# Optimization experiments

Hardware: AMD Instinct MI355X
Metric: run time of the kernel (lower is better)

## Reference

```python
import jax, jax.numpy as jnp
import numpy as np

B, T, ENC_C = 64, 512, 512   # batch, encoder frames, encoder channels
H = 512                      # hidden_channels
D = 80                       # out_channels (mel dim)
RF = 2                       # reduction_factor
PRE_IN = D * RF              # prenet input (= D*2, see go_frame)
PRE_INNER = 256
CONV_CH = 32                 # location conv channels
K = 31                       # location conv kernel size


def setup_inputs():
    key = jax.random.key(0)
    ks = jax.random.split(key, 16)
    s = 0.02
    f32 = jnp.float32
    p = {}
    p['enc_output'] = jax.random.normal(ks[0], (B, T, ENC_C), f32)
    # acoustic lengths in [T, 2T], multiples of RF -> len//RF in [T//2, T]
    p['data_len'] = (jax.random.randint(ks[1], (B,), T // 2, T + 1, jnp.int32) * RF).astype(jnp.int32)
    # Prenet: two 1x1 convs (== linears) + ReLU
    p['pn_w1'] = jax.random.normal(ks[2], (PRE_INNER, PRE_IN), f32) * s
    p['pn_b1'] = jnp.zeros((PRE_INNER,), f32)
    p['pn_w2'] = jax.random.normal(ks[3], (H, PRE_INNER), f32) * s
    p['pn_b2'] = jnp.zeros((H,), f32)
    # Location-sensitive attention
    p['att_enc_w'] = jax.random.normal(ks[4], (H, ENC_C), f32) * s
    p['att_enc_b'] = jnp.zeros((H,), f32)
    p['att_dec_w'] = jax.random.normal(ks[5], (H, H), f32) * s
    p['att_conv_w'] = jax.random.normal(ks[6], (CONV_CH, 1, K), f32) * s
    p['att_loc_w'] = jax.random.normal(ks[7], (H, CONV_CH), f32) * s
    p['att_v_w'] = jax.random.normal(ks[8], (H,), f32) * s
    p['att_v_b'] = jnp.zeros((), f32)
    # 2 GRU cells (torch GRUCell layout: gates [r|z|n])
    p['gru0_wih'] = jax.random.normal(ks[9], (3 * H, ENC_C + H), f32) * s
    p['gru0_whh'] = jax.random.normal(ks[10], (3 * H, H), f32) * s
    p['gru0_bih'] = jnp.zeros((3 * H,), f32)
    p['gru0_bhh'] = jnp.zeros((3 * H,), f32)
    p['gru1_wih'] = jax.random.normal(ks[11], (3 * H, H), f32) * s
    p['gru1_whh'] = jax.random.normal(ks[12], (3 * H, H), f32) * s
    p['gru1_bih'] = jnp.zeros((3 * H,), f32)
    p['gru1_bhh'] = jnp.zeros((3 * H,), f32)
    # out_layer: 1x1 Conv1d(2H -> D*RF) == linear
    p['out_w'] = jax.random.normal(ks[13], (D * RF, 2 * H), f32) * s
    p['out_b'] = jnp.zeros((D * RF,), f32)
    return p


def _gru(x, h, wih, whh, bih, bhh):
    gi = x @ wih.T + bih
    gh = h @ whh.T + bhh
    ir, iz, inn = jnp.split(gi, 3, axis=-1)
    hr, hz, hn = jnp.split(gh, 3, axis=-1)
    r = jax.nn.sigmoid(ir + hr)
    z = jax.nn.sigmoid(iz + hz)
    n = jnp.tanh(inn + r * hn)
    return (1.0 - z) * n + z * h


def _decode(enc_output, data_len, pn_w1, pn_b1, pn_w2, pn_b2,
            att_enc_w, att_enc_b, att_dec_w, att_conv_w, att_loc_w, att_v_w, att_v_b,
            gru0_wih, gru0_whh, gru0_bih, gru0_bhh,
            gru1_wih, gru1_whh, gru1_bih, gru1_bhh, out_w, out_b):
    dt = enc_output.dtype
    len_r = data_len // RF                                   # (B,) encoder-frame lengths
    pad = jnp.arange(T)[None, :] >= len_r[:, None]           # (B,T) True at padding
    valid = (~pad).astype(dt)
    att_prev0 = valid / len_r.astype(dt)[:, None]            # uniform init attention
    # processed memory (computed once, as in attention.reset_state caching)
    pm = jnp.einsum('btc,hc->bth', enc_output, att_enc_w) + att_enc_b

    def step(carry, t):
        h0, h1, prev_out, att_sum = carry
        prev_w = jnp.where(t == 0, att_prev0, att_sum)       # (B,T)
        # location features: 1D conv over previous (cumulative) attention
        f = jax.lax.conv_general_dilated(prev_w[:, None, :], att_conv_w,
                                         (1,), [(K // 2, K // 2)])  # (B,CONV_CH,T)
        loc = jnp.einsum('bct,hc->bth', f, att_loc_w)
        dec = (h0 @ att_dec_w.T)[:, None, :]                 # query from GRU layer 0 state
        erg = jnp.tanh(loc + pm + dec) @ att_v_w + att_v_b   # (B,T)
        erg = jnp.where(pad, jnp.asarray(-1e9, dt), erg)
        att_w = jax.nn.softmax(erg, axis=-1)
        att_c = jnp.einsum('bt,btc->bc', att_w, enc_output)  # context (B,ENC_C)
        # prenet (dropout in eval == identity)
        x = jax.nn.relu(prev_out @ pn_w1.T + pn_b1)
        x = jax.nn.relu(x @ pn_w2.T + pn_b2)
        h0n = _gru(jnp.concatenate([x, att_c], -1), h0, gru0_wih, gru0_whh, gru0_bih, gru0_bhh)
        h1n = _gru(h0n, h1, gru1_wih, gru1_whh, gru1_bih, gru1_bhh)
        out = jnp.concatenate([h1n, att_c], -1) @ out_w.T + out_b   # (B, D*RF)
        return (h0n, h1n, out, att_sum + att_w), (out, att_w)

    zeros = lambda *s: jnp.zeros(s, dt)
    carry0 = (zeros(B, H), zeros(B, H), zeros(B, D * RF), zeros(B, T))
    _, (outs, att_ws) = jax.lax.scan(step, carry0, jnp.arange(T))
    # outs: (T,B,D*RF); each step reshapes to (B,D,RF) and cats on time
    out = outs.transpose(1, 0, 2).reshape(B, T, D, RF).transpose(0, 2, 1, 3).reshape(B, D, T * RF)
    att_w = att_ws.transpose(1, 2, 0)                        # (B, T, T_steps)
    return out, att_w


def reference(enc_output, data_len, pn_w1, pn_b1, pn_w2, pn_b2,
              att_enc_w, att_enc_b, att_dec_w, att_conv_w, att_loc_w, att_v_w, att_v_b,
              gru0_wih, gru0_whh, gru0_bih, gru0_bhh,
              gru1_wih, gru1_whh, gru1_bih, gru1_bhh, out_w, out_b):
    return _decode(enc_output, data_len, pn_w1, pn_b1, pn_w2, pn_b2,
                   att_enc_w, att_enc_b, att_dec_w, att_conv_w, att_loc_w, att_v_w, att_v_b,
                   gru0_wih, gru0_whh, gru0_bih, gru0_bhh,
                   gru1_wih, gru1_whh, gru1_bih, gru1_bhh, out_w, out_b)
```

## Files before the change

kernel.cpp:

```cpp
#include <hip/hip_runtime.h>
#include <hip/hip_bf16.h>

typedef unsigned short u16;


__device__ __forceinline__ float b2f(u16 u) {
  return __uint_as_float(((unsigned)u) << 16);
}
__device__ __forceinline__ u16 f2b(float f) {
  unsigned u = __float_as_uint(f);
  u += 0x7fffu + ((u >> 16) & 1u);
  return (u16)(u >> 16);
}
template<bool F32>
__device__ __forceinline__ float ldw(const void* p, size_t i) {
  return F32 ? ((const float*)p)[i] : b2f(((const u16*)p)[i]);
}
template<bool F32>
__device__ __forceinline__ float4 ldw4(const void* p, size_t i) {
  if (F32) {
    return *(const float4*)((const float*)p + i);
  } else {
    uint2 u = *(const uint2*)((const u16*)p + i);
    float4 r;
    r.x = __uint_as_float(u.x << 16);
    r.y = __uint_as_float(u.x & 0xffff0000u);
    r.z = __uint_as_float(u.y << 16);
    r.w = __uint_as_float(u.y & 0xffff0000u);
    return r;
  }
}
template<bool F32>
__device__ __forceinline__ void stout(void* p, size_t i, float v) {
  if (F32) ((float*)p)[i] = v; else ((u16*)p)[i] = f2b(v);
}
__device__ __forceinline__ float frcp(float x) { return __builtin_amdgcn_rcpf(x); }
__device__ __forceinline__ float tanh_f(float x) {
  float e = __expf(2.f * x);
  return 1.f - 2.f * frcp(e + 1.f);
}
__device__ __forceinline__ float sig_f(float x) { return frcp(1.f + __expf(-x)); }

__device__ __forceinline__ void st_sc(int* p, int v) {
  __hip_atomic_store(p, v, __ATOMIC_RELAXED, __HIP_MEMORY_SCOPE_AGENT);
}
__device__ __forceinline__ int ld_sc(const int* p) {
  return __hip_atomic_load(p, __ATOMIC_RELAXED, __HIP_MEMORY_SCOPE_AGENT);
}
__device__ __forceinline__ void stf_sc(float* p, float v) {
  __hip_atomic_store(p, v, __ATOMIC_RELAXED, __HIP_MEMORY_SCOPE_AGENT);
}
__device__ __forceinline__ float ldf_sc(const float* p) {
  return __hip_atomic_load(p, __ATOMIC_RELAXED, __HIP_MEMORY_SCOPE_AGENT);
}

__device__ __forceinline__ void stage_n(float* lds, const float* src, int n, int tid) {
  int i = 0;
  for (; i + 8192 <= n; i += 8192) {
    float r[16];
#pragma unroll
    for (int j = 0; j < 16; ++j) r[j] = ldf_sc(src + i + tid + j * 512);
#pragma unroll
    for (int j = 0; j < 16; ++j) lds[i + tid + j * 512] = r[j];
  }
  for (; i < n; i += 2048) {
    float r[4];
#pragma unroll
    for (int j = 0; j < 4; ++j) r[j] = ldf_sc(src + i + tid + j * 512);
#pragma unroll
    for (int j = 0; j < 4; ++j) lds[i + tid + j * 512] = r[j];
  }
}

template<bool F32, int NR>
__device__ __forceinline__ void dotN(float* __restrict__ acc, const float* __restrict__ sb,
                                     const void* __restrict__ wb, size_t rb, int wstride,
                                     int nk, int lane, int vz) {
  float4 wa[NR], wn[NR];
#pragma unroll
  for (int i = 0; i < NR; ++i) wa[i] = ldw4<F32>(wb, rb + (size_t)i * wstride + vz);
  for (int kg = 0; kg < nk; kg += 8) {
#pragma unroll
    for (int i = 0; i < NR; ++i) wn[i] = ldw4<F32>(wb, rb + (size_t)i * wstride + kg + 4 + vz);
    float a0 = sb[(kg + 0) * 64 + lane], a1 = sb[(kg + 1) * 64 + lane],
          a2 = sb[(kg + 2) * 64 + lane], a3 = sb[(kg + 3) * 64 + lane];
#pragma unroll
    for (int i = 0; i < NR; ++i)
      acc[i] = fmaf(wa[i].w, a3, fmaf(wa[i].z, a2, fmaf(wa[i].y, a1, fmaf(wa[i].x, a0, acc[i]))));
    int kn = (kg + 8 < nk) ? kg + 8 : kg;
#pragma unroll
    for (int i = 0; i < NR; ++i) wa[i] = ldw4<F32>(wb, rb + (size_t)i * wstride + kn + vz);
    float b0 = sb[(kg + 4) * 64 + lane], b1 = sb[(kg + 5) * 64 + lane],
          b2 = sb[(kg + 6) * 64 + lane], b3 = sb[(kg + 7) * 64 + lane];
#pragma unroll
    for (int i = 0; i < NR; ++i)
      acc[i] = fmaf(wn[i].w, b3, fmaf(wn[i].z, b2, fmaf(wn[i].y, b1, fmaf(wn[i].x, b0, acc[i]))));
  }
}

constexpr size_t OBAR  = 0;
constexpr size_t OFLG  = OBAR  + 128;
constexpr size_t OASUM = OFLG  + 8192;
constexpr size_t ODEC  = OASUM + 32768;
constexpr size_t OH0   = ODEC  + 32768;
constexpr size_t OH1   = OH0   + 32768;
constexpr size_t OPO   = OH1   + 32768;
constexpr size_t OZEND = OPO   + 10240;
constexpr int    ZERO_SPAN_N = (int)OZEND;
constexpr size_t OPRV  = OZEND;
constexpr size_t OERG  = OPRV  + 32768;
constexpr size_t OX1   = OERG  + 32768;
constexpr size_t OX2   = OX1   + 16384;
constexpr size_t OATTC = OX2   + 32768;
constexpr size_t OMM   = OATTC + 32768;
constexpr size_t OGI0  = OMM   + 16384;
constexpr size_t OGH0  = OGI0  + 393216;
constexpr size_t OGH1  = OGH0  + 196608;
constexpr size_t OGI1  = OGH1  + 196608;
constexpr size_t OPM   = OGI1  + 393216;
constexpr size_t OTOT  = OPM   + 8388608;

__device__ __forceinline__ void fastbar(int* flags, int* gen, int target,
                                        int wg, int tid) {
  __syncthreads();
  if (tid == 0) st_sc(flags + wg * 32, target);
  if (wg == 0) {
    if (tid < 64) {
      int i0 = tid * 4;
      for (;;) {
        int ok = (ld_sc(flags + (i0 + 0) * 32) >= target)
               & (ld_sc(flags + (i0 + 1) * 32) >= target)
               & (ld_sc(flags + (i0 + 2) * 32) >= target)
               & (ld_sc(flags + (i0 + 3) * 32) >= target);
        if (__ballot(ok) == 0xFFFFFFFFFFFFFFFFull) break;
      }
      if (tid == 0) st_sc(gen, target);
    }
    __syncthreads();
  } else {
    if (tid == 0) {
      while (ld_sc(gen) < target) {}
    }
    __syncthreads();
  }
}

__global__ void k_zero(float* p, int n) {
  for (int i = blockIdx.x * 256 + threadIdx.x; i < n; i += gridDim.x * 256) p[i] = 0.f;
}
__global__ void k_detect(int* flag, const u16* probe) {
  if (blockIdx.x != 0 || threadIdx.x != 0) return;
  int sane = 0;
  for (int i = 0; i < 256; i += 2) {
    u16 u = probe[i];
    int e = (u >> 7) & 0xFF;
    if (u == 0 || (e >= 97 && e <= 140)) ++sane;
  }
  *flag = (sane < 96) ? 1 : 0;
}
__global__ void k_prevw(float* prevw, const int* dlen) {
  int b = blockIdx.x;
  int len = dlen[b] >> 1;
  float inv = 1.f / (float)len;
  for (int i = threadIdx.x; i < 512; i += 256)
    prevw[b * 512 + i] = (i < len) ? inv : 0.f;
}
template<bool F32>
__global__ void k_cvtT512(const int* flag, float* dst, const void* src) {
  if (*flag != (F32 ? 1 : 0)) return;
  for (int i = blockIdx.x * 256 + threadIdx.x; i < 262144; i += gridDim.x * 256) {
    int c = i >> 9, h = i & 511;
    dst[i] = ldw<F32>(src, (size_t)h * 512 + c);
  }
}
template<bool F32>
__global__ void k_mmat(const int* flag, float* M, const void* locw, const void* convw) {
  if (*flag != (F32 ? 1 : 0)) return;
  int i = blockIdx.x * 256 + threadIdx.x;
  if (i >= 16384) return;
  int h = i >> 5, k = i & 31;
  float acc = 0.f;
  if (k < 31) {
    for (int c = 0; c < 32; ++c)
      acc = fmaf(ldw<F32>(locw, h * 32 + c), ldw<F32>(convw, c * 31 + k), acc);
  }
  M[i] = acc;
}
template<bool F32>
__global__ __launch_bounds__(256) void k_pm(const int* flag, u16* pm, const void* enc,
                                            const float* encwT, const void* encb) {
  if (*flag != (F32 ? 1 : 0)) return;
  __shared__ float encf[16 * 512];
  int row0 = blockIdx.x * 16;
  int tid = threadIdx.x;
  for (int i = tid; i < 16 * 512; i += 256) {
    int r = i >> 9, c = i & 511;
    encf[i] = ldw<F32>(enc, (size_t)(row0 + r) * 512 + c);
  }
  __syncthreads();
  float a0[16], a1[16];
  float bb0 = ldw<F32>(encb, tid), bb1 = ldw<F32>(encb, tid + 256);
#pragma unroll
  for (int r = 0; r < 16; ++r) { a0[r] = bb0; a1[r] = bb1; }
  for (int c = 0; c < 512; ++c) {
    float w0 = encwT[c * 512 + tid];
    float w1 = encwT[c * 512 + 256 + tid];
#pragma unroll
    for (int r = 0; r < 16; ++r) {
      float a = encf[r * 512 + c];
      a0[r] = fmaf(w0, a, a0[r]);
      a1[r] = fmaf(w1, a, a1[r]);
    }
  }
#pragma unroll
  for (int r = 0; r < 16; ++r) {
    pm[(size_t)(row0 + r) * 512 + tid]       = f2b(a0[r]);
    pm[(size_t)(row0 + r) * 512 + 256 + tid] = f2b(a1[r]);
  }
}

struct KP {
  const void* __restrict__ enc;
  const int* __restrict__ dlen;
  const u16* __restrict__ pm;
  const void* __restrict__ wih0; const void* __restrict__ whh0;
  const void* __restrict__ wih1; const void* __restrict__ whh1;
  const void* __restrict__ adec; const void* __restrict__ outw;
  const void* __restrict__ pnw2; const void* __restrict__ pnw1;
  const void* __restrict__ pnb1; const void* __restrict__ pnb2;
  const void* __restrict__ bih0; const void* __restrict__ bhh0;
  const void* __restrict__ bih1; const void* __restrict__ bhh1;
  const void* __restrict__ outb; const void* __restrict__ vw;
  const float* __restrict__ Mg;
  int* __restrict__ bar;
  int* __restrict__ flags;
  float* __restrict__ asum; float* __restrict__ dec;
  float* __restrict__ h0T;  float* __restrict__ h1T;  float* __restrict__ poT;
  float* __restrict__ prevw; float* __restrict__ erg;
  float* __restrict__ x1T;  float* __restrict__ x2T;  float* __restrict__ attcT;
  float* __restrict__ gi0p; float* __restrict__ gh0p;
  float* __restrict__ gh1p; float* __restrict__ gi1p;
  void* __restrict__ out;
};

template<bool F32>
__global__ __launch_bounds__(512, 2) void k_loop(KP p) {
  if (*(const volatile int*)(p.bar + 64) != (F32 ? 1 : 0)) return;
  __shared__ float stg[16384];
  __shared__ u16  M_u[32 * 512];
  __shared__ float dec_s[512];
  __shared__ float v_s[512];
  __shared__ float wq[160];
  __shared__ float sm[512];
  __shared__ float red[16];

  const int wg = blockIdx.x, tid = threadIdx.x;
  const int lane = tid & 63;
  const int wv = __builtin_amdgcn_readfirstlane(tid >> 6);
  const int b_att = wg >> 2, q = wg & 3, t0 = q * 128;
  const int trow = tid >> 6;
  const int hcol = tid & 63;
  float* dec1 = p.gh0p;
  int* genp = p.bar + 32;
  int bt = 0;
  int vz;
  asm volatile("v_mov_b32 %0, 0" : "=v"(vz));

  for (int i = tid; i < 32 * 512; i += 512) {
    int k = i >> 9, h = i & 511;
    M_u[i] = f2b(p.Mg[h * 32 + k]);
  }
  if (tid < 512) v_s[tid] = ldw<F32>(p.vw, tid);
  __syncthreads();

  for (int t = 0; t < 512; ++t) {
    if (wg < 32) stage_n(stg, p.poT, 10240, tid);
    if (tid < 158) {
      int g = t0 - 15 + tid;
      wq[tid] = (g >= 0 && g < 512) ? ldf_sc(p.prevw + b_att * 512 + g) : 0.f;
    }
    if (tid < 512)
      dec_s[tid] = ldf_sc(p.dec + b_att * 512 + tid) + ldf_sc(dec1 + b_att * 512 + tid);
    __syncthreads();
    if (wg < 32) {
      int n = wg * 8 + wv;
      float a[1] = {0.f};
      dotN<F32, 1>(a, stg, p.pnw1, (size_t)n * 160, 160, 160, lane, vz);
      stf_sc(p.x1T + n * 64 + lane, fmaxf(a[0] + ldw<F32>(p.pnb1, n), 0.f));
    }
    {
      float wreg[46];
#pragma unroll
      for (int i = 0; i < 46; ++i) wreg[i] = wq[trow * 16 + i];
      float acc[16];
#pragma unroll
      for (int s = 0; s < 16; ++s) acc[s] = 0.f;
      const u16* pmb = p.pm + ((size_t)(b_att * 512 + t0 + trow * 16)) * 512;
      for (int j = 0; j < 8; ++j) {
        int hj = hcol + 64 * j;
        float Mreg[31];
#pragma unroll
        for (int k = 0; k < 31; ++k) Mreg[k] = b2f(M_u[k * 512 + hj]);
        float dj = dec_s[hj], vj = v_s[hj];
#pragma unroll
        for (int s = 0; s < 16; ++s) {
          float u = dj;
#pragma unroll
          for (int k = 0; k < 31; ++k) u = fmaf(Mreg[k], wreg[s + k], u);
          u += b2f(pmb[s * 512 + hj]);
          acc[s] = fmaf(vj, tanh_f(u), acc[s]);
        }
      }
#pragma unroll
      for (int s = 0; s < 16; ++s) {
        float v = acc[s];
#pragma unroll
        for (int off = 32; off; off >>= 1) v += __shfl_xor(v, off, 64);
        if (hcol == 0) sm[trow * 16 + s] = v;
      }
      __syncthreads();
      if (tid < 128) stf_sc(p.erg + b_att * 512 + t0 + tid, sm[tid]);
    }
    fastbar(p.flags, genp, ++bt, wg, tid);

    if (wg < 64) {
      int b = wg;
      int len = p.dlen[b] >> 1;
      float e0 = ldf_sc(p.erg + b * 512 + tid);
      bool v0 = tid < len;
      float mx = v0 ? e0 : -1e30f;
#pragma unroll
      for (int off = 32; off; off >>= 1) mx = fmaxf(mx, __shfl_xor(mx, off, 64));
      if (lane == 0) red[wv] = mx;
      __syncthreads();
      mx = fmaxf(fmaxf(fmaxf(red[0], red[1]), fmaxf(red[2], red[3])),
                 fmaxf(fmaxf(red[4], red[5]), fmaxf(red[6], red[7])));
      float x0 = v0 ? __expf(e0 - mx) : 0.f;
      float s = x0;
#pragma unroll
      for (int off = 32; off; off >>= 1) s += __shfl_xor(s, off, 64);
      if (lane == 0) red[8 + wv] = s;
      __syncthreads();
      s = ((red[8] + red[9]) + (red[10] + red[11])) + ((red[12] + red[13]) + (red[14] + red[15]));
      float w0 = x0 * frcp(s);
      stout<F32>(p.out, 5242880 + (size_t)b * 262144 + (size_t)tid * 512 + t, w0);
      float s0 = p.asum[b * 512 + tid] + w0;
      p.asum[b * 512 + tid] = s0;
      stf_sc(p.prevw + b * 512 + tid, s0);
    } else if (wg < 192) {
      int idx = wg - 64, b = idx >> 1, half = idx & 1;
      int len = p.dlen[b] >> 1;
      float e0 = ldf_sc(p.erg + b * 512 + tid);
      bool v0 = tid < len;
      float mx = v0 ? e0 : -1e30f;
#pragma unroll
      for (int off = 32; off; off >>= 1) mx = fmaxf(mx, __shfl_xor(mx, off, 64));
      if (lane == 0) red[wv] = mx;
      __syncthreads();
      mx = fmaxf(fmaxf(fmaxf(red[0], red[1]), fmaxf(red[2], red[3])),
                 fmaxf(fmaxf(red[4], red[5]), fmaxf(red[6], red[7])));
      float x0 = v0 ? __expf(e0 - mx) : 0.f;
      float s = x0;
#pragma unroll
      for (int off = 32; off; off >>= 1) s += __shfl_xor(s, off, 64);
      if (lane == 0) red[8 + wv] = s;
      __syncthreads();
      s = ((red[8] + red[9]) + (red[10] + red[11])) + ((red[12] + red[13]) + (red[14] + red[15]));
      sm[tid] = x0 * frcp(s);
      __syncthreads();
      int c4 = half * 256 + lane * 4;
      size_t eb = (size_t)b * 262144 + c4;
      float4 ac[16];
#pragma unroll
      for (int i = 0; i < 16; ++i) ac[i] = make_float4(0.f, 0.f, 0.f, 0.f);
      int tb = wv * 64;
      for (int tt = 0; tt < 64; tt += 16) {
#pragma unroll
        for (int i = 0; i < 16; ++i) {
          float4 e = ldw4<F32>(p.enc, eb + (size_t)(tb + tt + i) * 512);
          float w = sm[tb + tt + i];
          ac[i].x = fmaf(w, e.x, ac[i].x);
          ac[i].y = fmaf(w, e.y, ac[i].y);
          ac[i].z = fmaf(w, e.z, ac[i].z);
          ac[i].w = fmaf(w, e.w, ac[i].w);
        }
      }
      float4 ssum;
      ssum.x = 0.f; ssum.y = 0.f; ssum.z = 0.f; ssum.w = 0.f;
#pragma unroll
      for (int i = 0; i < 16; ++i) {
        ssum.x += ac[i].x; ssum.y += ac[i].y; ssum.z += ac[i].z; ssum.w += ac[i].w;
      }
      __syncthreads();
      *(float4*)&stg[wv * 256 + lane * 4] = ssum;
      __syncthreads();
      if (tid < 256) {
        float r = ((stg[tid] + stg[256 + tid]) + (stg[512 + tid] + stg[768 + tid]))
                + ((stg[1024 + tid] + stg[1280 + tid]) + (stg[1536 + tid] + stg[1792 + tid]));
        stf_sc(p.attcT + (half * 256 + tid) * 64 + b, r);
      }
    } else {
      stage_n(stg, p.x1T, 16384, tid);
      __syncthreads();
      int idx = wg - 192;
      int n = idx * 8 + wv;
      float a[1] = {0.f};
      dotN<F32, 1>(a, stg, p.pnw2, (size_t)n * 256, 256, 256, lane, vz);
      stf_sc(p.x2T + n * 64 + lane, fmaxf(a[0] + ldw<F32>(p.pnb2, n), 0.f));
    }
    fastbar(p.flags, genp, ++bt, wg, tid);

    {
      const float* src; const void* wb; float* dst;
      int n0, wstride, wc0;
      if (wg < 128) {
        int kpart = wg & 3, ngrp = wg >> 2;
        src = ((kpart < 2) ? p.x2T : p.attcT) + (kpart & 1) * 16384;
        wb = p.wih0; wstride = 1024;
        wc0 = (kpart >> 1) * 512 + (kpart & 1) * 256;
        n0 = ngrp * 48 + wv * 6;
        dst = p.gi0p + ((size_t)kpart * 1536 + n0) * 64;
      } else if (wg < 192) {
        int idx = wg - 128, kpart = idx & 1, ngrp = idx >> 1;
        src = p.h0T + kpart * 16384;
        wb = p.whh0; wstride = 512; wc0 = kpart * 256;
        n0 = ngrp * 48 + wv * 6;
        dst = p.gh0p + ((size_t)kpart * 1536 + n0) * 64;
      } else {
        int idx = wg - 192, kpart = idx & 1, ngrp = idx >> 1;
        src = p.h1T + kpart * 16384;
        wb = p.whh1; wstride = 512; wc0 = kpart * 256;
        n0 = ngrp * 48 + wv * 6;
        dst = p.gh1p + ((size_t)kpart * 1536 + n0) * 64;
      }
      stage_n(stg, src, 16384, tid);
      __syncthreads();
      float acc[6];
#pragma unroll
      for (int i = 0; i < 6; ++i) acc[i] = 0.f;
      dotN<F32, 6>(acc, stg, wb, (size_t)n0 * wstride + wc0, wstride, 256, lane, vz);
#pragma unroll
      for (int i = 0; i < 6; ++i) stf_sc(dst + (size_t)i * 64 + lane, acc[i]);
    }
    fastbar(p.flags, genp, ++bt, wg, tid);

    if (wg < 64) {
      int e = wg * 512 + tid;
      int h = e >> 6, b = e & 63;
      float ir = ldf_sc(p.gi0p + h * 64 + b) + ldf_sc(p.gi0p + (1536 + h) * 64 + b)
               + ldf_sc(p.gi0p + (3072 + h) * 64 + b) + ldf_sc(p.gi0p + (4608 + h) * 64 + b)
               + ldw<F32>(p.bih0, h);
      float iz = ldf_sc(p.gi0p + (512 + h) * 64 + b) + ldf_sc(p.gi0p + (2048 + h) * 64 + b)
               + ldf_sc(p.gi0p + (3584 + h) * 64 + b) + ldf_sc(p.gi0p + (5120 + h) * 64 + b)
               + ldw<F32>(p.bih0, 512 + h);
      float in = ldf_sc(p.gi0p + (1024 + h) * 64 + b) + ldf_sc(p.gi0p + (2560 + h) * 64 + b)
               + ldf_sc(p.gi0p + (4096 + h) * 64 + b) + ldf_sc(p.gi0p + (5632 + h) * 64 + b)
               + ldw<F32>(p.bih0, 1024 + h);
      float hr = ldf_sc(p.gh0p + h * 64 + b) + ldf_sc(p.gh0p + (1536 + h) * 64 + b)
               + ldw<F32>(p.bhh0, h);
      float hz = ldf_sc(p.gh0p + (512 + h) * 64 + b) + ldf_sc(p.gh0p + (2048 + h) * 64 + b)
               + ldw<F32>(p.bhh0, 512 + h);
      float hn = ldf_sc(p.gh0p + (1024 + h) * 64 + b) + ldf_sc(p.gh0p + (2560 + h) * 64 + b)
               + ldw<F32>(p.bhh0, 1024 + h);
      float r = sig_f(ir + hr), z = sig_f(iz + hz);
      float nn = tanh_f(in + r * hn);
      float ho = ldf_sc(p.h0T + h * 64 + b);
      stf_sc(p.h0T + h * 64 + b, (1.f - z) * nn + z * ho);
    }
    fastbar(p.flags, genp, ++bt, wg, tid);

    if (wg < 128) {
      int kpart = wg & 3, ngrp = wg >> 2;
      stage_n(stg, p.h0T + kpart * 8192, 8192, tid);
      __syncthreads();
      int n0 = ngrp * 48 + wv * 6;
      float acc[6];
#pragma unroll
      for (int i = 0; i < 6; ++i) acc[i] = 0.f;
      dotN<F32, 6>(acc, stg, p.wih1, (size_t)n0 * 512 + kpart * 128, 512, 128, lane, vz);
#pragma unroll
      for (int i = 0; i < 6; ++i)
        stf_sc(p.gi1p + ((size_t)kpart * 1536 + n0 + i) * 64 + lane, acc[i]);
    } else {
      int g = wg - 128;
      int cpart = g >> 6;
      int n = (g & 63) * 8 + wv;
      stage_n(stg, p.h0T + cpart * 16384, 16384, tid);
      __syncthreads();
      float r[1] = {0.f};
      dotN<F32, 1>(r, stg, p.adec, (size_t)n * 512 + cpart * 256, 512, 256, lane, vz);
      float* dst = cpart ? dec1 : p.dec;
      stf_sc(dst + lane * 512 + n, r[0]);
    }
    fastbar(p.flags, genp, ++bt, wg, tid);

    if (wg < 64) {
      int e = wg * 512 + tid;
      int h = e >> 6, b = e & 63;
      float ir = ldf_sc(p.gi1p + h * 64 + b) + ldf_sc(p.gi1p + (1536 + h) * 64 + b)
               + ldf_sc(p.gi1p + (3072 + h) * 64 + b) + ldf_sc(p.gi1p + (4608 + h) * 64 + b)
               + ldw<F32>(p.bih1, h);
      float iz = ldf_sc(p.gi1p + (512 + h) * 64 + b) + ldf_sc(p.gi1p + (2048 + h) * 64 + b)
               + ldf_sc(p.gi1p + (3584 + h) * 64 + b) + ldf_sc(p.gi1p + (5120 + h) * 64 + b)
               + ldw<F32>(p.bih1, 512 + h);
      float in = ldf_sc(p.gi1p + (1024 + h) * 64 + b) + ldf_sc(p.gi1p + (2560 + h) * 64 + b)
               + ldf_sc(p.gi1p + (4096 + h) * 64 + b) + ldf_sc(p.gi1p + (5632 + h) * 64 + b)
               + ldw<F32>(p.bih1, 1024 + h);
      float hr = ldf_sc(p.gh1p + h * 64 + b) + ldf_sc(p.gh1p + (1536 + h) * 64 + b)
               + ldw<F32>(p.bhh1, h);
      float hz = ldf_sc(p.gh1p + (512 + h) * 64 + b) + ldf_sc(p.gh1p + (2048 + h) * 64 + b)
               + ldw<F32>(p.bhh1, 512 + h);
      float hn = ldf_sc(p.gh1p + (1024 + h) * 64 + b) + ldf_sc(p.gh1p + (2560 + h) * 64 + b)
               + ldw<F32>(p.bhh1, 1024 + h);
      float r = sig_f(ir + hr), z = sig_f(iz + hz);
      float nn = tanh_f(in + r * hn);
      float ho = ldf_sc(p.h1T + h * 64 + b);
      stf_sc(p.h1T + h * 64 + b, (1.f - z) * nn + z * ho);
    }
    fastbar(p.flags, genp, ++bt, wg, tid);

    if (wg < 20) {
      int n = wg * 8 + wv;
      float r[1] = {0.f};
      for (int c = 0; c < 4; ++c) {
        const float* src = ((c < 2) ? p.h1T : p.attcT) + (c & 1) * 16384;
        stage_n(stg, src, 16384, tid);
        __syncthreads();
        dotN<F32, 1>(r, stg, p.outw, (size_t)n * 1024 + c * 256, 1024, 256, lane, vz);
        __syncthreads();
      }
      float acc = r[0] + ldw<F32>(p.outb, n);
      stf_sc(p.poT + n * 64 + lane, acc);
      stout<F32>(p.out, (size_t)lane * 81920 + (size_t)(n >> 1) * 1024 + t * 2 + (n & 1), acc);
    }
    fastbar(p.flags, genp, ++bt, wg, tid);
  }
}

extern "C" void kernel_launch(void* const* d_in, const int* in_sizes, int n_in,
                              void* d_out, int out_size, void* d_ws, size_t ws_size,
                              hipStream_t stream) {
  (void)in_sizes; (void)n_in; (void)out_size; (void)ws_size;
  const void* enc   = d_in[0];
  const int*  dlen  = (const int*)d_in[1];
  const void* pnw1  = d_in[2];
  const void* pnb1  = d_in[3];
  const void* pnw2  = d_in[4];
  const void* pnb2  = d_in[5];
  const void* aencw = d_in[6];
  const void* aencb = d_in[7];
  const void* adecw = d_in[8];
  const void* aconv = d_in[9];
  const void* alocw = d_in[10];
  const void* avw   = d_in[11];
  const void* wih0  = d_in[13];
  const void* whh0  = d_in[14];
  const void* bih0  = d_in[15];
  const void* bhh0  = d_in[16];
  const void* wih1  = d_in[17];
  const void* whh1  = d_in[18];
  const void* bih1  = d_in[19];
  const void* bhh1  = d_in[20];
  const void* outw  = d_in[21];
  const void* outb  = d_in[22];

  float* W = (float*)d_ws;
  int* flag = (int*)(W + OBAR) + 64;
  dim3 blk(256);

  k_zero<<<256, blk, 0, stream>>>(W + OBAR, ZERO_SPAN_N);
  k_zero<<<64, blk, 0, stream>>>(W + OGH0, 32768);
  k_detect<<<1, blk, 0, stream>>>(flag, (const u16*)pnw1);
  k_prevw<<<64, blk, 0, stream>>>(W + OPRV, dlen);
  k_mmat<false><<<64, blk, 0, stream>>>(flag, W + OMM, alocw, aconv);
  k_mmat<true ><<<64, blk, 0, stream>>>(flag, W + OMM, alocw, aconv);
  k_cvtT512<false><<<512, blk, 0, stream>>>(flag, W + OGI0, aencw);
  k_cvtT512<true ><<<512, blk, 0, stream>>>(flag, W + OGI0, aencw);
  k_pm<false><<<2048, blk, 0, stream>>>(flag, (u16*)(W + OPM), enc, W + OGI0, aencb);
  k_pm<true ><<<2048, blk, 0, stream>>>(flag, (u16*)(W + OPM), enc, W + OGI0, aencb);

  KP kp;
  kp.enc = enc; kp.dlen = dlen;
  kp.pm = (const u16*)(W + OPM);
  kp.wih0 = wih0; kp.whh0 = whh0;
  kp.wih1 = wih1; kp.whh1 = whh1;
  kp.adec = adecw; kp.outw = outw;
  kp.pnw2 = pnw2; kp.pnw1 = pnw1;
  kp.pnb1 = pnb1; kp.pnb2 = pnb2;
  kp.bih0 = bih0; kp.bhh0 = bhh0;
  kp.bih1 = bih1; kp.bhh1 = bhh1;
  kp.outb = outb; kp.vw = avw;
  kp.Mg = W + OMM;
  kp.bar = (int*)(W + OBAR);
  kp.flags = (int*)(W + OFLG);
  kp.asum = W + OASUM; kp.dec = W + ODEC;
  kp.h0T = W + OH0; kp.h1T = W + OH1; kp.poT = W + OPO;
  kp.prevw = W + OPRV; kp.erg = W + OERG;
  kp.x1T = W + OX1; kp.x2T = W + OX2; kp.attcT = W + OATTC;
  kp.gi0p = W + OGI0; kp.gh0p = W + OGH0;
  kp.gh1p = W + OGH1; kp.gi1p = W + OGI1;
  kp.out = d_out;

  k_loop<false><<<dim3(256), dim3(512), 0, stream>>>(kp);
  k_loop<true ><<<dim3(256), dim3(512), 0, stream>>>(kp);
}
```

Baseline: 99.31 ms.

## Vectorize cross-workgroup staging and GRU loads, transpose projected-memory layout

Replaces the scalar coherent LDS staging loops with dwordx4 loads that bypass caches (sc0 sc1), issued in a batch and then waited on once. The GRU gate phases now use 16 workgroups that each handle 4 batch lanes with vectorized loads and stores, instead of 64 workgroups doing scalar work. The projected encoder memory is stored transposed (h-major, time contiguous) so the attention energy loop reads 16 bf16 values with two 128-bit loads. The intent is fewer memory instructions and less latency in the serialized per-step phases. The cost is hand-written inline asm with manual waitcnt handling and fewer active workgroups in the GRU phases.

```diff
diff --git a/kernel.cpp b/kernel.cpp
--- a/kernel.cpp
+++ b/kernel.cpp
@@ -2,6 +2,7 @@
 #include <hip/hip_bf16.h>
 
 typedef unsigned short u16;
+typedef float f32x4 __attribute__((ext_vector_type(4)));
 
 
 __device__ __forceinline__ float b2f(u16 u) {
@@ -54,22 +55,25 @@
   return __hip_atomic_load(p, __ATOMIC_RELAXED, __HIP_MEMORY_SCOPE_AGENT);
 }
 
-__device__ __forceinline__ void stage_n(float* lds, const float* src, int n, int tid) {
-  int i = 0;
-  for (; i + 8192 <= n; i += 8192) {
-    float r[16];
-#pragma unroll
-    for (int j = 0; j < 16; ++j) r[j] = ldf_sc(src + i + tid + j * 512);
-#pragma unroll
-    for (int j = 0; j < 16; ++j) lds[i + tid + j * 512] = r[j];
-  }
-  for (; i < n; i += 2048) {
-    float r[4];
-#pragma unroll
-    for (int j = 0; j < 4; ++j) r[j] = ldf_sc(src + i + tid + j * 512);
-#pragma unroll
-    for (int j = 0; j < 4; ++j) lds[i + tid + j * 512] = r[j];
-  }
+__device__ __forceinline__ void ld4_sc_issue(f32x4* dst, const float* p) {
+  asm volatile("global_load_dwordx4 %0, %1, off sc0 sc1" : "=v"(*dst) : "v"(p));
+}
+__device__ __forceinline__ void vm_wait0() {
+  asm volatile("s_waitcnt vmcnt(0)" ::: "memory");
+  __builtin_amdgcn_sched_barrier(0);
+}
+__device__ __forceinline__ void st4_sc(float* p, f32x4 v) {
+  asm volatile("global_store_dwordx4 %0, %1, off sc0 sc1" :: "v"(p), "v"(v) : "memory");
+}
+
+template<int NB>
+__device__ __forceinline__ void stage4(float* lds, const float* src, int tid) {
+  f32x4 r[NB];
+#pragma unroll
+  for (int j = 0; j < NB; ++j) ld4_sc_issue(&r[j], src + j * 2048 + tid * 4);
+  vm_wait0();
+#pragma unroll
+  for (int j = 0; j < NB; ++j) *(f32x4*)&lds[j * 2048 + tid * 4] = r[j];
 }
 
 template<bool F32, int NR>
@@ -212,11 +216,19 @@
       a1[r] = fmaf(w1, a, a1[r]);
     }
   }
-#pragma unroll
-  for (int r = 0; r < 16; ++r) {
-    pm[(size_t)(row0 + r) * 512 + tid]       = f2b(a0[r]);
-    pm[(size_t)(row0 + r) * 512 + 256 + tid] = f2b(a1[r]);
-  }
+  int b = row0 >> 9, tl0 = row0 & 511;
+  unsigned w0p[8], w1p[8];
+#pragma unroll
+  for (int rr = 0; rr < 8; ++rr) {
+    w0p[rr] = (unsigned)f2b(a0[2 * rr]) | ((unsigned)f2b(a0[2 * rr + 1]) << 16);
+    w1p[rr] = (unsigned)f2b(a1[2 * rr]) | ((unsigned)f2b(a1[2 * rr + 1]) << 16);
+  }
+  uint4* d0 = (uint4*)(pm + ((size_t)(b * 512 + tid)) * 512 + tl0);
+  d0[0] = make_uint4(w0p[0], w0p[1], w0p[2], w0p[3]);
+  d0[1] = make_uint4(w0p[4], w0p[5], w0p[6], w0p[7]);
+  uint4* d1 = (uint4*)(pm + ((size_t)(b * 512 + 256 + tid)) * 512 + tl0);
+  d1[0] = make_uint4(w1p[0], w1p[1], w1p[2], w1p[3]);
+  d1[1] = make_uint4(w1p[4], w1p[5], w1p[6], w1p[7]);
 }
 
 struct KP {
@@ -274,13 +286,21 @@
   __syncthreads();
 
   for (int t = 0; t < 512; ++t) {
-    if (wg < 32) stage_n(stg, p.poT, 10240, tid);
+    if (wg < 32) stage4<5>(stg, p.poT, tid);
     if (tid < 158) {
       int g = t0 - 15 + tid;
       wq[tid] = (g >= 0 && g < 512) ? ldf_sc(p.prevw + b_att * 512 + g) : 0.f;
     }
-    if (tid < 512)
-      dec_s[tid] = ldf_sc(p.dec + b_att * 512 + tid) + ldf_sc(dec1 + b_att * 512 + tid);
+    if (tid < 128) {
+      f32x4 da, db;
+      ld4_sc_issue(&da, p.dec + b_att * 512 + tid * 4);
+      ld4_sc_issue(&db, dec1 + b_att * 512 + tid * 4);
+      vm_wait0();
+      dec_s[tid * 4 + 0] = da[0] + db[0];
+      dec_s[tid * 4 + 1] = da[1] + db[1];
+      dec_s[tid * 4 + 2] = da[2] + db[2];
+      dec_s[tid * 4 + 3] = da[3] + db[3];
+    }
     __syncthreads();
     if (wg < 32) {
       int n = wg * 8 + wv;
@@ -295,19 +315,23 @@
       float acc[16];
 #pragma unroll
       for (int s = 0; s < 16; ++s) acc[s] = 0.f;
-      const u16* pmb = p.pm + ((size_t)(b_att * 512 + t0 + trow * 16)) * 512;
+      const u16* pmTb = p.pm + ((size_t)(b_att * 512)) * 512 + t0 + trow * 16;
       for (int j = 0; j < 8; ++j) {
         int hj = hcol + 64 * j;
         float Mreg[31];
 #pragma unroll
         for (int k = 0; k < 31; ++k) Mreg[k] = b2f(M_u[k * 512 + hj]);
         float dj = dec_s[hj], vj = v_s[hj];
+        const uint4* rp = (const uint4*)(pmTb + (size_t)hj * 512);
+        uint4 q0 = rp[0], q1 = rp[1];
+        unsigned qa[8] = {q0.x, q0.y, q0.z, q0.w, q1.x, q1.y, q1.z, q1.w};
 #pragma unroll
         for (int s = 0; s < 16; ++s) {
           float u = dj;
 #pragma unroll
           for (int k = 0; k < 31; ++k) u = fmaf(Mreg[k], wreg[s + k], u);
-          u += b2f(pmb[s * 512 + hj]);
+          unsigned wbits = qa[s >> 1];
+          u += (s & 1) ? __uint_as_float(wbits & 0xffff0000u) : __uint_as_float(wbits << 16);
           acc[s] = fmaf(vj, tanh_f(u), acc[s]);
         }
       }
@@ -400,7 +424,7 @@
         stf_sc(p.attcT + (half * 256 + tid) * 64 + b, r);
       }
     } else {
-      stage_n(stg, p.x1T, 16384, tid);
+      stage4<8>(stg, p.x1T, tid);
       __syncthreads();
       int idx = wg - 192;
       int n = idx * 8 + wv;
@@ -433,7 +457,7 @@
         n0 = ngrp * 48 + wv * 6;
         dst = p.gh1p + ((size_t)kpart * 1536 + n0) * 64;
       }
-      stage_n(stg, src, 16384, tid);
+      stage4<8>(stg, src, tid);
       __syncthreads();
       float acc[6];
 #pragma unroll
@@ -444,34 +468,44 @@
     }
     fastbar(p.flags, genp, ++bt, wg, tid);
 
-    if (wg < 64) {
+    if (wg < 16) {
       int e = wg * 512 + tid;
-      int h = e >> 6, b = e & 63;
-      float ir = ldf_sc(p.gi0p + h * 64 + b) + ldf_sc(p.gi0p + (1536 + h) * 64 + b)
-               + ldf_sc(p.gi0p + (3072 + h) * 64 + b) + ldf_sc(p.gi0p + (4608 + h) * 64 + b)
-               + ldw<F32>(p.bih0, h);
-      float iz = ldf_sc(p.gi0p + (512 + h) * 64 + b) + ldf_sc(p.gi0p + (2048 + h) * 64 + b)
-               + ldf_sc(p.gi0p + (3584 + h) * 64 + b) + ldf_sc(p.gi0p + (5120 + h) * 64 + b)
-               + ldw<F32>(p.bih0, 512 + h);
-      float in = ldf_sc(p.gi0p + (1024 + h) * 64 + b) + ldf_sc(p.gi0p + (2560 + h) * 64 + b)
-               + ldf_sc(p.gi0p + (4096 + h) * 64 + b) + ldf_sc(p.gi0p + (5632 + h) * 64 + b)
-               + ldw<F32>(p.bih0, 1024 + h);
-      float hr = ldf_sc(p.gh0p + h * 64 + b) + ldf_sc(p.gh0p + (1536 + h) * 64 + b)
-               + ldw<F32>(p.bhh0, h);
-      float hz = ldf_sc(p.gh0p + (512 + h) * 64 + b) + ldf_sc(p.gh0p + (2048 + h) * 64 + b)
-               + ldw<F32>(p.bhh0, 512 + h);
-      float hn = ldf_sc(p.gh0p + (1024 + h) * 64 + b) + ldf_sc(p.gh0p + (2560 + h) * 64 + b)
-               + ldw<F32>(p.bhh0, 1024 + h);
-      float r = sig_f(ir + hr), z = sig_f(iz + hz);
-      float nn = tanh_f(in + r * hn);
-      float ho = ldf_sc(p.h0T + h * 64 + b);
-      stf_sc(p.h0T + h * 64 + b, (1.f - z) * nn + z * ho);
+      int h = e >> 4, b0 = (e & 15) * 4;
+      f32x4 gi[12], gh[6], h0v;
+#pragma unroll
+      for (int c = 0; c < 4; ++c)
+#pragma unroll
+        for (int g3 = 0; g3 < 3; ++g3)
+          ld4_sc_issue(&gi[c * 3 + g3], p.gi0p + ((size_t)c * 1536 + g3 * 512 + h) * 64 + b0);
+#pragma unroll
+      for (int c = 0; c < 2; ++c)
+#pragma unroll
+        for (int g3 = 0; g3 < 3; ++g3)
+          ld4_sc_issue(&gh[c * 3 + g3], p.gh0p + ((size_t)c * 1536 + g3 * 512 + h) * 64 + b0);
+      ld4_sc_issue(&h0v, p.h0T + h * 64 + b0);
+      float bi_r = ldw<F32>(p.bih0, h), bi_z = ldw<F32>(p.bih0, 512 + h), bi_n = ldw<F32>(p.bih0, 1024 + h);
+      float bh_r = ldw<F32>(p.bhh0, h), bh_z = ldw<F32>(p.bhh0, 512 + h), bh_n = ldw<F32>(p.bhh0, 1024 + h);
+      vm_wait0();
+      f32x4 outv;
+#pragma unroll
+      for (int qq = 0; qq < 4; ++qq) {
+        float ir = bi_r + gi[0][qq] + gi[3][qq] + gi[6][qq] + gi[9][qq];
+        float iz = bi_z + gi[1][qq] + gi[4][qq] + gi[7][qq] + gi[10][qq];
+        float in = bi_n + gi[2][qq] + gi[5][qq] + gi[8][qq] + gi[11][qq];
+        float hr = bh_r + gh[0][qq] + gh[3][qq];
+        float hz = bh_z + gh[1][qq] + gh[4][qq];
+        float hn = bh_n + gh[2][qq] + gh[5][qq];
+        float r = sig_f(ir + hr), z = sig_f(iz + hz);
+        float nn = tanh_f(in + r * hn);
+        outv[qq] = (1.f - z) * nn + z * h0v[qq];
+      }
+      st4_sc(p.h0T + h * 64 + b0, outv);
     }
     fastbar(p.flags, genp, ++bt, wg, tid);
 
     if (wg < 128) {
       int kpart = wg & 3, ngrp = wg >> 2;
-      stage_n(stg, p.h0T + kpart * 8192, 8192, tid);
+      stage4<4>(stg, p.h0T + kpart * 8192, tid);
       __syncthreads();
       int n0 = ngrp * 48 + wv * 6;
       float acc[6];
@@ -485,7 +519,7 @@
       int g = wg - 128;
       int cpart = g >> 6;
       int n = (g & 63) * 8 + wv;
-      stage_n(stg, p.h0T + cpart * 16384, 16384, tid);
+      stage4<8>(stg, p.h0T + cpart * 16384, tid);
       __syncthreads();
       float r[1] = {0.f};
       dotN<F32, 1>(r, stg, p.adec, (size_t)n * 512 + cpart * 256, 512, 256, lane, vz);
@@ -494,28 +528,38 @@
     }
     fastbar(p.flags, genp, ++bt, wg, tid);
 
-    if (wg < 64) {
+    if (wg < 16) {
       int e = wg * 512 + tid;
-      int h = e >> 6, b = e & 63;
-      float ir = ldf_sc(p.gi1p + h * 64 + b) + ldf_sc(p.gi1p + (1536 + h) * 64 + b)
-               + ldf_sc(p.gi1p + (3072 + h) * 64 + b) + ldf_sc(p.gi1p + (4608 + h) * 64 + b)
-               + ldw<F32>(p.bih1, h);
-      float iz = ldf_sc(p.gi1p + (512 + h) * 64 + b) + ldf_sc(p.gi1p + (2048 + h) * 64 + b)
-               + ldf_sc(p.gi1p + (3584 + h) * 64 + b) + ldf_sc(p.gi1p + (5120 + h) * 64 + b)
-               + ldw<F32>(p.bih1, 512 + h);
-      float in = ldf_sc(p.gi1p + (1024 + h) * 64 + b) + ldf_sc(p.gi1p + (2560 + h) * 64 + b)
-               + ldf_sc(p.gi1p + (4096 + h) * 64 + b) + ldf_sc(p.gi1p + (5632 + h) * 64 + b)
-               + ldw<F32>(p.bih1, 1024 + h);
-      float hr = ldf_sc(p.gh1p + h * 64 + b) + ldf_sc(p.gh1p + (1536 + h) * 64 + b)
-               + ldw<F32>(p.bhh1, h);
-      float hz = ldf_sc(p.gh1p + (512 + h) * 64 + b) + ldf_sc(p.gh1p + (2048 + h) * 64 + b)
-               + ldw<F32>(p.bhh1, 512 + h);
-      float hn = ldf_sc(p.gh1p + (1024 + h) * 64 + b) + ldf_sc(p.gh1p + (2560 + h) * 64 + b)
-               + ldw<F32>(p.bhh1, 1024 + h);
-      float r = sig_f(ir + hr), z = sig_f(iz + hz);
-      float nn = tanh_f(in + r * hn);
-      float ho = ldf_sc(p.h1T + h * 64 + b);
-      stf_sc(p.h1T + h * 64 + b, (1.f - z) * nn + z * ho);
+      int h = e >> 4, b0 = (e & 15) * 4;
+      f32x4 gi[12], gh[6], h1v;
+#pragma unroll
+      for (int c = 0; c < 4; ++c)
+#pragma unroll
+        for (int g3 = 0; g3 < 3; ++g3)
+          ld4_sc_issue(&gi[c * 3 + g3], p.gi1p + ((size_t)c * 1536 + g3 * 512 + h) * 64 + b0);
+#pragma unroll
+      for (int c = 0; c < 2; ++c)
+#pragma unroll
+        for (int g3 = 0; g3 < 3; ++g3)
+          ld4_sc_issue(&gh[c * 3 + g3], p.gh1p + ((size_t)c * 1536 + g3 * 512 + h) * 64 + b0);
+      ld4_sc_issue(&h1v, p.h1T + h * 64 + b0);
+      float bi_r = ldw<F32>(p.bih1, h), bi_z = ldw<F32>(p.bih1, 512 + h), bi_n = ldw<F32>(p.bih1, 1024 + h);
+      float bh_r = ldw<F32>(p.bhh1, h), bh_z = ldw<F32>(p.bhh1, 512 + h), bh_n = ldw<F32>(p.bhh1, 1024 + h);
+      vm_wait0();
+      f32x4 outv;
+#pragma unroll
+      for (int qq = 0; qq < 4; ++qq) {
+        float ir = bi_r + gi[0][qq] + gi[3][qq] + gi[6][qq] + gi[9][qq];
+        float iz = bi_z + gi[1][qq] + gi[4][qq] + gi[7][qq] + gi[10][qq];
+        float in = bi_n + gi[2][qq] + gi[5][qq] + gi[8][qq] + gi[11][qq];
+        float hr = bh_r + gh[0][qq] + gh[3][qq];
+        float hz = bh_z + gh[1][qq] + gh[4][qq];
+        float hn = bh_n + gh[2][qq] + gh[5][qq];
+        float r = sig_f(ir + hr), z = sig_f(iz + hz);
+        float nn = tanh_f(in + r * hn);
+        outv[qq] = (1.f - z) * nn + z * h1v[qq];
+      }
+      st4_sc(p.h1T + h * 64 + b0, outv);
     }
     fastbar(p.flags, genp, ++bt, wg, tid);
 
@@ -524,7 +568,7 @@
       float r[1] = {0.f};
       for (int c = 0; c < 4; ++c) {
         const float* src = ((c < 2) ? p.h1T : p.attcT) + (c & 1) * 16384;
-        stage_n(stg, src, 16384, tid);
+        stage4<8>(stg, src, tid);
         __syncthreads();
         dotN<F32, 1>(r, stg, p.outw, (size_t)n * 1024 + c * 256, 1024, 256, lane, vz);
         __syncthreads();
```

Result: faster. 86.81 ms (-12.6%).
